# Kernel tuning notes

Hardware: AMD Instinct MI355X
Metric: run time of the kernel (lower is better)

The kernel has to match this reference:

```python
import jax, jax.numpy as jnp
import numpy as np

EPS = 1e-5
NEG_SLOPE = 0.01  # F.leaky_relu default


def setup_inputs() -> dict:
    key = jax.random.key(0)
    k1, k2, k3, k4 = jax.random.split(key, 4)
    N, F, H = 8192, 512, 2
    inputs = jax.random.normal(k1, (N, F), dtype=jnp.float32)
    adj = jnp.zeros((N, N), dtype=jnp.float32)  # accepted but unused by the module
    # torch Linear(F, F*H, bias=False): y = x @ W with W of shape [F, F*H]
    W = jax.random.normal(k2, (F, F * H), dtype=jnp.float32) * (1.0 / np.sqrt(F))
    a_w = jax.random.normal(k3, (1,), dtype=jnp.float32)  # Linear(1,1) weight
    a_b = jax.random.normal(k4, (1,), dtype=jnp.float32)  # Linear(1,1) bias
    return {"inputs": inputs, "adj": adj, "W": W, "a_w": a_w, "a_b": a_b}


def reference(inputs, adj, W, a_w, a_b):
    # Wh, Ws = chunk(inputs @ W, 2)
    WhWs = inputs @ W                       # [N, 2F]
    Wh, Ws = jnp.split(WhWs, 2, axis=-1)    # each [N, F]
    # bias = a(ones) = a_w * 1 + a_b  (constant scalar broadcast)
    bias = (a_w + a_b)[0]
    # dense attention: tanh(Wh + Ws + bias) @ Wh^T  -> [N, N]
    scores = jnp.tanh(Wh + Ws + bias) @ Wh.T
    attn = jax.nn.softmax(scores, axis=-1)  # [N, N]
    out = attn @ Wh + inputs                # [N, F] residual
    # training-mode batch norm over node dim, no affine
    mean = jnp.mean(out, axis=0)
    var = jnp.var(out, axis=0)
    out = (out - mean) * jax.lax.rsqrt(var + EPS)
    return jnp.where(out >= 0, out, NEG_SLOPE * out)
```

## Files before the change

kernel.cpp:

```cpp
#include <hip/hip_runtime.h>

using f32x4 = float    __attribute__((ext_vector_type(4)));
using f16x8 = _Float16 __attribute__((ext_vector_type(8)));
using f16x4 = _Float16 __attribute__((ext_vector_type(4)));

__device__ __forceinline__ void gload_lds16(const void* g, void* l) {
    __builtin_amdgcn_global_load_lds(
        (__attribute__((address_space(1))) void*)(void*)g,
        (__attribute__((address_space(3))) void*)l, 16, 0, 0);
}


__global__ __launch_bounds__(256) void k_cvt_x(
    const float* __restrict__ in, _Float16* __restrict__ out) {
    int i = (blockIdx.x * 256 + threadIdx.x) * 8;
    f32x4 a = *(const f32x4*)(in + i);
    f32x4 b = *(const f32x4*)(in + i + 4);
    f16x8 o;
    #pragma unroll
    for (int j = 0; j < 4; ++j) { o[j] = (_Float16)a[j]; o[j + 4] = (_Float16)b[j]; }
    *(f16x8*)(out + i) = o;
}

__global__ __launch_bounds__(256) void k_cvtT(
    const float* __restrict__ in, _Float16* __restrict__ out, int R, int C) {
    __shared__ _Float16 tile[32][33];
    int c0 = blockIdx.x * 32, r0 = blockIdx.y * 32;
    int tx = threadIdx.x & 31, ty = threadIdx.x >> 5;
    #pragma unroll
    for (int i = ty; i < 32; i += 8)
        tile[i][tx] = (_Float16)in[(size_t)(r0 + i) * C + c0 + tx];
    __syncthreads();
    #pragma unroll
    for (int i = ty; i < 32; i += 8)
        out[(size_t)(c0 + i) * R + r0 + tx] = tile[tx][i];
}

__global__ __launch_bounds__(512, 4) void k_gemm1f(
    const _Float16* __restrict__ A, const _Float16* __restrict__ Bt,
    _Float16* __restrict__ Whh, _Float16* __restrict__ T,
    _Float16* __restrict__ WhT,
    const float* __restrict__ aw, const float* __restrict__ ab) {
    __shared__ _Float16 As[128 * 32];
    __shared__ _Float16 B0s[64 * 32];
    __shared__ _Float16 B1s[64 * 32];
    const float bias = aw[0] + ab[0];
    const int row0 = blockIdx.y * 128, col0 = blockIdx.x * 64;
    const int tid = threadIdx.x, w = tid >> 6, lane = tid & 63;
    const int wm = w >> 2, wn = w & 3;
    const int lrow = lane & 15, quad = lane >> 4;
    const int r16 = lane >> 2;
    const int kc = (((lane & 3) - ((lane >> 3) & 3)) & 3) * 8;
    const int sq = ((quad + ((lrow >> 1) & 3)) & 3) * 8;
    f32x4 acc0[4] = {}, acc1[4] = {};
    for (int k0 = 0; k0 < 512; k0 += 32) {
        gload_lds16(A + (size_t)(row0 + w * 16 + r16) * 512 + k0 + kc,
                    As + w * 512);
        if (w < 4)
            gload_lds16(Bt + (size_t)(col0 + w * 16 + r16) * 512 + k0 + kc,
                        B0s + w * 512);
        else
            gload_lds16(Bt + (size_t)(col0 + 512 + (w - 4) * 16 + r16) * 512 + k0 + kc,
                        B1s + (w - 4) * 512);
        __syncthreads();
        f16x8 af[4], b0, b1;
        #pragma unroll
        for (int i = 0; i < 4; ++i)
            af[i] = *(const f16x8*)(As + (wm * 64 + i * 16 + lrow) * 32 + sq);
        b0 = *(const f16x8*)(B0s + (wn * 16 + lrow) * 32 + sq);
        b1 = *(const f16x8*)(B1s + (wn * 16 + lrow) * 32 + sq);
        #pragma unroll
        for (int mi = 0; mi < 4; ++mi) {
            acc0[mi] = __builtin_amdgcn_mfma_f32_16x16x32_f16(af[mi], b0, acc0[mi], 0, 0, 0);
            acc1[mi] = __builtin_amdgcn_mfma_f32_16x16x32_f16(af[mi], b1, acc1[mi], 0, 0, 0);
        }
        __syncthreads();
    }
    const int col = col0 + wn * 16 + lrow;
    #pragma unroll
    for (int mi = 0; mi < 4; ++mi) {
        int rowb = row0 + wm * 64 + mi * 16 + quad * 4;
        f16x4 pw;
        #pragma unroll
        for (int r = 0; r < 4; ++r) {
            float wh = acc0[mi][r];
            float tt = tanhf(wh + acc1[mi][r] + bias);
            Whh[(size_t)(rowb + r) * 512 + col] = (_Float16)wh;
            T[(size_t)(rowb + r) * 512 + col]   = (_Float16)tt;
            pw[r] = (_Float16)wh;
        }
        *(f16x4*)(WhT + (size_t)col * 8192 + rowb) = pw;
    }
}

__global__ __launch_bounds__(512, 4) void k_gemm2(
    const _Float16* __restrict__ A,
    const _Float16* __restrict__ Bt,
    _Float16* __restrict__ Cp,
    float* __restrict__ msP, float* __restrict__ lsP) {
    __shared__ _Float16 As[256 * 64];
    __shared__ _Float16 Bs[128 * 64];
    const int row0 = blockIdx.y * 256, col0 = blockIdx.x * 128;
    const int tid = threadIdx.x, w = tid >> 6, lane = tid & 63;
    const int wm = w >> 1, wn = w & 1;
    const int lrow = lane & 15, quad = lane >> 4;
    const int r8 = lane >> 3;
    const int kc8 = (((lane & 7) - r8) & 7) * 8;
    f32x4 acc[4][4] = {};
    for (int k0 = 0; k0 < 512; k0 += 64) {
        #pragma unroll
        for (int i = 0; i < 6; ++i) {
            int c = w + i * 8;
            if (c < 32) {
                gload_lds16(A + (size_t)(row0 + c * 8 + r8) * 512 + k0 + kc8,
                            As + c * 512);
            } else {
                int c2 = c - 32;
                gload_lds16(Bt + (size_t)(col0 + c2 * 8 + r8) * 512 + k0 + kc8,
                            Bs + c2 * 512);
            }
        }
        __syncthreads();
        #pragma unroll
        for (int ks = 0; ks < 2; ++ks) {
            const int sl = ((quad + ks * 4 + lrow) & 7) * 8;
            f16x8 af[4], bf[4];
            #pragma unroll
            for (int i = 0; i < 4; ++i)
                af[i] = *(const f16x8*)(As + (wm * 64 + i * 16 + lrow) * 64 + sl);
            #pragma unroll
            for (int i = 0; i < 4; ++i)
                bf[i] = *(const f16x8*)(Bs + (wn * 64 + i * 16 + lrow) * 64 + sl);
            #pragma unroll
            for (int mi = 0; mi < 4; ++mi)
                #pragma unroll
                for (int ni = 0; ni < 4; ++ni)
                    acc[mi][ni] = __builtin_amdgcn_mfma_f32_16x16x32_f16(
                        af[mi], bf[ni], acc[mi][ni], 0, 0, 0);
        }
        __syncthreads();
    }
    const int cb = blockIdx.x * 2 + wn;
    #pragma unroll
    for (int mi = 0; mi < 4; ++mi) {
        #pragma unroll
        for (int r = 0; r < 4; ++r) {
            const int row = row0 + wm * 64 + mi * 16 + quad * 4 + r;
            float vq[4]; float sm = -3.0e38f;
            #pragma unroll
            for (int ni = 0; ni < 4; ++ni) {
                _Float16 hv = (_Float16)acc[mi][ni][r];
                Cp[(size_t)row * 8192 + col0 + wn * 64 + ni * 16 + lrow] = hv;
                vq[ni] = (float)hv;
                sm = fmaxf(sm, vq[ni]);
            }
            #pragma unroll
            for (int off = 1; off < 16; off <<= 1)
                sm = fmaxf(sm, __shfl_xor(sm, off));
            float ls = 0.f;
            #pragma unroll
            for (int ni = 0; ni < 4; ++ni) ls += __expf(vq[ni] - sm);
            #pragma unroll
            for (int off = 1; off < 16; off <<= 1)
                ls += __shfl_xor(ls, off);
            if (lrow == 0) {
                msP[(size_t)cb * 8192 + row] = sm;
                lsP[(size_t)cb * 8192 + row] = ls;
            }
        }
    }
}

__global__ __launch_bounds__(64) void k_rowstats(
    const float* __restrict__ ms, const float* __restrict__ ls,
    float* __restrict__ mrow, float* __restrict__ rl) {
    const int row = blockIdx.x * 64 + threadIdx.x;
    float m[8], l[8];
    #pragma unroll
    for (int k = 0; k < 8; ++k) { m[k] = -3.0e38f; l[k] = 0.f; }
    for (int j = 0; j < 16; ++j) {
        #pragma unroll
        for (int k = 0; k < 8; ++k) {
            const int cb = k * 16 + j;
            float mb = ms[(size_t)cb * 8192 + row];
            float lb = ls[(size_t)cb * 8192 + row];
            float mn = fmaxf(m[k], mb);
            l[k] = l[k] * __expf(m[k] - mn) + lb * __expf(mb - mn);
            m[k] = mn;
        }
    }
    float M = m[0];
    #pragma unroll
    for (int k = 1; k < 8; ++k) M = fmaxf(M, m[k]);
    float L = 0.f;
    #pragma unroll
    for (int k = 0; k < 8; ++k) L += l[k] * __expf(m[k] - M);
    mrow[row] = M * 1.44269504f;
    rl[row]   = 1.f / L;
}

__global__ __launch_bounds__(512, 4) void k_gemm3(
    const _Float16* __restrict__ A,
    const _Float16* __restrict__ Bt,
    const float* __restrict__ mrow,
    float* __restrict__ Cp) {
    __shared__ _Float16 As[128 * 64];
    __shared__ _Float16 Bs[256 * 64];
    const int row0 = blockIdx.y * 128, col0 = blockIdx.x * 256;
    const size_t zoff = (size_t)blockIdx.z * 2048;
    Cp += (size_t)blockIdx.z * ((size_t)8192 * 512);
    const int tid = threadIdx.x, w = tid >> 6, lane = tid & 63;
    const int wm = w >> 2, wn = w & 3;
    const int lrow = lane & 15, quad = lane >> 4;
    const int r8 = lane >> 3;
    const int kc8 = (((lane & 7) - r8) & 7) * 8;
    const int rowA0 = row0 + w * 8 + r8;
    const int rowA1 = row0 + (w + 8) * 8 + r8;
    const float ms0 = mrow[rowA0];
    const float ms1 = mrow[rowA1];
    f32x4 acc[4][4] = {};
    for (int k0 = 0; k0 < 2048; k0 += 64) {
        f16x8 h0 = *(const f16x8*)(A + (size_t)rowA0 * 8192 + zoff + k0 + kc8);
        f16x8 h1 = *(const f16x8*)(A + (size_t)rowA1 * 8192 + zoff + k0 + kc8);
        f16x8 q0, q1;
        #pragma unroll
        for (int j = 0; j < 8; ++j) {
            q0[j] = (_Float16)exp2f(fmaf((float)h0[j], 1.44269504f, -ms0));
            q1[j] = (_Float16)exp2f(fmaf((float)h1[j], 1.44269504f, -ms1));
        }
        *(f16x8*)(As + w * 512 + lane * 8)       = q0;
        *(f16x8*)(As + (w + 8) * 512 + lane * 8) = q1;
        #pragma unroll
        for (int i = 2; i < 6; ++i) {
            int c2 = w + i * 8 - 16;
            gload_lds16(Bt + (size_t)(col0 + c2 * 8 + r8) * 8192 + zoff + k0 + kc8,
                        Bs + c2 * 512);
        }
        __syncthreads();
        #pragma unroll
        for (int ks = 0; ks < 2; ++ks) {
            const int sl = ((quad + ks * 4 + lrow) & 7) * 8;
            f16x8 af[4], bf[4];
            #pragma unroll
            for (int i = 0; i < 4; ++i)
                af[i] = *(const f16x8*)(As + (wm * 64 + i * 16 + lrow) * 64 + sl);
            #pragma unroll
            for (int i = 0; i < 4; ++i)
                bf[i] = *(const f16x8*)(Bs + (wn * 64 + i * 16 + lrow) * 64 + sl);
            #pragma unroll
            for (int mi = 0; mi < 4; ++mi)
                #pragma unroll
                for (int ni = 0; ni < 4; ++ni)
                    acc[mi][ni] = __builtin_amdgcn_mfma_f32_16x16x32_f16(
                        af[mi], bf[ni], acc[mi][ni], 0, 0, 0);
        }
        __syncthreads();
    }
    #pragma unroll
    for (int mi = 0; mi < 4; ++mi) {
        #pragma unroll
        for (int ni = 0; ni < 4; ++ni) {
            int col = col0 + wn * 64 + ni * 16 + lrow;
            #pragma unroll
            for (int r = 0; r < 4; ++r) {
                int row = row0 + wm * 64 + mi * 16 + quad * 4 + r;
                Cp[(size_t)row * 512 + col] = acc[mi][ni][r];
            }
        }
    }
}

__global__ __launch_bounds__(256) void k_reduce_stats(
    const float* __restrict__ part, const float* __restrict__ X,
    const float* __restrict__ rl,
    float* __restrict__ outf, float* __restrict__ cs, float* __restrict__ cq) {
    const int t = threadIdx.x;
    const int r0 = blockIdx.x * 32;
    constexpr size_t PS = (size_t)8192 * 512;
    float s0 = 0, q0 = 0, s1 = 0, q1 = 0;
    for (int r = 0; r < 32; ++r) {
        size_t base = (size_t)(r0 + r) * 512;
        float rlv = rl[r0 + r];
        float a = (part[base + t] + part[PS + base + t]
                + part[2 * PS + base + t] + part[3 * PS + base + t]) * rlv
                + X[base + t];
        float b = (part[base + t + 256] + part[PS + base + t + 256]
                + part[2 * PS + base + t + 256] + part[3 * PS + base + t + 256]) * rlv
                + X[base + t + 256];
        outf[base + t] = a;       outf[base + t + 256] = b;
        s0 += a; q0 += a * a; s1 += b; q1 += b * b;
    }
    atomicAdd(&cs[t], s0);       atomicAdd(&cq[t], q0);
    atomicAdd(&cs[t + 256], s1); atomicAdd(&cq[t + 256], q1);
}

__global__ __launch_bounds__(256) void k_bn_lrelu(
    const float* __restrict__ outf, const float* __restrict__ colsum,
    const float* __restrict__ colsq, float* __restrict__ out) {
    int i = blockIdx.x * 256 + threadIdx.x;
    int c = i & 511;
    constexpr float rN = 1.f / 8192.f;
    float mean = colsum[c] * rN;
    float var  = colsq[c] * rN - mean * mean;
    float y = (outf[i] - mean) * rsqrtf(var + 1e-5f);
    y = (y >= 0.f) ? y : 0.01f * y;
    out[i] = y;
}

extern "C" void kernel_launch(void* const* d_in, const int* in_sizes, int n_in,
                              void* d_out, int out_size, void* d_ws, size_t ws_size,
                              hipStream_t stream) {
    const float* X  = (const float*)d_in[0];
    const float* W  = (const float*)d_in[2];
    const float* aw = (const float*)d_in[3];
    const float* ab = (const float*)d_in[4];
    float* out = (float*)d_out;

    char* ws = (char*)d_ws;
    _Float16* Xh   = (_Float16*)(ws + 0x0);
    _Float16* Wt   = (_Float16*)(ws + 0x800000);
    _Float16* T    = (_Float16*)(ws + 0x900000);
    _Float16* Whh  = (_Float16*)(ws + 0x1100000);
    _Float16* WhT  = (_Float16*)(ws + 0x1900000);
    _Float16* S    = (_Float16*)(ws + 0x2100000);
    float*    outf = (float*)   (ws + 0xA100000);
    float*    part = (float*)   (ws + 0xB100000);
    float*    msP  = (float*)   (ws + 0xB100000);
    float*    lsP  = (float*)   (ws + 0xB500000);
    float*    cs   = (float*)   (ws + 0xF100000);
    float*    cq   = (float*)   (ws + 0xF100800);
    float*    mrow = (float*)   (ws + 0xF101000);
    float*    rl   = (float*)   (ws + 0xF109000);

    hipMemsetAsync(cs, 0, 4096, stream);
    k_cvt_x<<<dim3((8192 * 512) / 2048), 256, 0, stream>>>(X, Xh);
    k_cvtT<<<dim3(1024 / 32, 512 / 32), 256, 0, stream>>>(W, Wt, 512, 1024);
    k_gemm1f<<<dim3(8, 64), 512, 0, stream>>>(Xh, Wt, Whh, T, WhT, aw, ab);
    k_gemm2<<<dim3(64, 32), 512, 0, stream>>>(T, Whh, S, msP, lsP);
    k_rowstats<<<dim3(128), 64, 0, stream>>>(msP, lsP, mrow, rl);
    k_gemm3<<<dim3(2, 64, 4), 512, 0, stream>>>(S, WhT, mrow, part);
    k_reduce_stats<<<dim3(256), 256, 0, stream>>>(part, X, rl, outf, cs, cq);
    k_bn_lrelu<<<dim3((8192 * 512) / 256), 256, 0, stream>>>(outf, cs, cq, out);
}
```

Baseline: 535.7 us.

## Move softmax denominator accumulation into the PV GEMM and simplify row stats

The gemm2 epilogue now records only per-block row maxima and no longer computes or stores partial exp sums. A simpler k_rowmax kernel reduces those maxima. The softmax denominators are summed inside k_gemm3 from the exponentials it already computes, and reduce_stats inverts them. The change also remaps gemm3 to a 1D grid with a swizzled block order for better L2 locality, and issues the B-tile async loads before the A exp work to overlap them.

```diff
diff --git a/kernel.cpp b/kernel.cpp
--- a/kernel.cpp
+++ b/kernel.cpp
@@ -97,7 +97,7 @@
     const _Float16* __restrict__ A,
     const _Float16* __restrict__ Bt,
     _Float16* __restrict__ Cp,
-    float* __restrict__ msP, float* __restrict__ lsP) {
+    float* __restrict__ msP) {
     __shared__ _Float16 As[256 * 64];
     __shared__ _Float16 Bs[128 * 64];
     const int row0 = blockIdx.y * 256, col0 = blockIdx.x * 128;
@@ -146,69 +146,51 @@
         #pragma unroll
         for (int r = 0; r < 4; ++r) {
             const int row = row0 + wm * 64 + mi * 16 + quad * 4 + r;
-            float vq[4]; float sm = -3.0e38f;
+            float sm = -3.0e38f;
             #pragma unroll
             for (int ni = 0; ni < 4; ++ni) {
                 _Float16 hv = (_Float16)acc[mi][ni][r];
                 Cp[(size_t)row * 8192 + col0 + wn * 64 + ni * 16 + lrow] = hv;
-                vq[ni] = (float)hv;
-                sm = fmaxf(sm, vq[ni]);
+                sm = fmaxf(sm, (float)hv);
             }
             #pragma unroll
             for (int off = 1; off < 16; off <<= 1)
                 sm = fmaxf(sm, __shfl_xor(sm, off));
-            float ls = 0.f;
-            #pragma unroll
-            for (int ni = 0; ni < 4; ++ni) ls += __expf(vq[ni] - sm);
-            #pragma unroll
-            for (int off = 1; off < 16; off <<= 1)
-                ls += __shfl_xor(ls, off);
-            if (lrow == 0) {
-                msP[(size_t)cb * 8192 + row] = sm;
-                lsP[(size_t)cb * 8192 + row] = ls;
-            }
-        }
-    }
-}
-
-__global__ __launch_bounds__(64) void k_rowstats(
-    const float* __restrict__ ms, const float* __restrict__ ls,
-    float* __restrict__ mrow, float* __restrict__ rl) {
-    const int row = blockIdx.x * 64 + threadIdx.x;
-    float m[8], l[8];
-    #pragma unroll
-    for (int k = 0; k < 8; ++k) { m[k] = -3.0e38f; l[k] = 0.f; }
-    for (int j = 0; j < 16; ++j) {
-        #pragma unroll
-        for (int k = 0; k < 8; ++k) {
-            const int cb = k * 16 + j;
-            float mb = ms[(size_t)cb * 8192 + row];
-            float lb = ls[(size_t)cb * 8192 + row];
-            float mn = fmaxf(m[k], mb);
-            l[k] = l[k] * __expf(m[k] - mn) + lb * __expf(mb - mn);
-            m[k] = mn;
-        }
-    }
-    float M = m[0];
-    #pragma unroll
-    for (int k = 1; k < 8; ++k) M = fmaxf(M, m[k]);
-    float L = 0.f;
-    #pragma unroll
-    for (int k = 0; k < 8; ++k) L += l[k] * __expf(m[k] - M);
+            if (lrow == 0) msP[(size_t)cb * 8192 + row] = sm;
+        }
+    }
+}
+
+__global__ __launch_bounds__(256) void k_rowmax(
+    const float* __restrict__ ms, float* __restrict__ mrow) {
+    const int row = blockIdx.x * 256 + threadIdx.x;
+    float m[8];
+    #pragma unroll
+    for (int k = 0; k < 8; ++k) m[k] = -3.0e38f;
+    #pragma unroll
+    for (int j = 0; j < 16; ++j)
+        #pragma unroll
+        for (int k = 0; k < 8; ++k)
+            m[k] = fmaxf(m[k], ms[(size_t)(j * 8 + k) * 8192 + row]);
+    float M = fmaxf(fmaxf(fmaxf(m[0], m[1]), fmaxf(m[2], m[3])),
+                    fmaxf(fmaxf(m[4], m[5]), fmaxf(m[6], m[7])));
     mrow[row] = M * 1.44269504f;
-    rl[row]   = 1.f / L;
 }
 
 __global__ __launch_bounds__(512, 4) void k_gemm3(
     const _Float16* __restrict__ A,
     const _Float16* __restrict__ Bt,
     const float* __restrict__ mrow,
-    float* __restrict__ Cp) {
+    float* __restrict__ Cp,
+    float* __restrict__ lpart) {
     __shared__ _Float16 As[128 * 64];
     __shared__ _Float16 Bs[256 * 64];
-    const int row0 = blockIdx.y * 128, col0 = blockIdx.x * 256;
-    const size_t zoff = (size_t)blockIdx.z * 2048;
-    Cp += (size_t)blockIdx.z * ((size_t)8192 * 512);
+    const int bid = blockIdx.x;
+    const int orig = ((bid & 7) << 6) | (bid >> 3);
+    const int bx = orig & 1, by = (orig >> 1) & 63, bz = orig >> 7;
+    const int row0 = by * 128, col0 = bx * 256;
+    const size_t zoff = (size_t)bz * 2048;
+    Cp += (size_t)bz * ((size_t)8192 * 512);
     const int tid = threadIdx.x, w = tid >> 6, lane = tid & 63;
     const int wm = w >> 2, wn = w & 3;
     const int lrow = lane & 15, quad = lane >> 4;
@@ -218,24 +200,29 @@
     const int rowA1 = row0 + (w + 8) * 8 + r8;
     const float ms0 = mrow[rowA0];
     const float ms1 = mrow[rowA1];
+    float lsum0 = 0.f, lsum1 = 0.f;
     f32x4 acc[4][4] = {};
     for (int k0 = 0; k0 < 2048; k0 += 64) {
+        #pragma unroll
+        for (int i = 0; i < 4; ++i) {
+            int c2 = w + i * 8;
+            gload_lds16(Bt + (size_t)(col0 + c2 * 8 + r8) * 8192 + zoff + k0 + kc8,
+                        Bs + c2 * 512);
+        }
         f16x8 h0 = *(const f16x8*)(A + (size_t)rowA0 * 8192 + zoff + k0 + kc8);
         f16x8 h1 = *(const f16x8*)(A + (size_t)rowA1 * 8192 + zoff + k0 + kc8);
         f16x8 q0, q1;
+        float e0 = 0.f, e1 = 0.f;
         #pragma unroll
         for (int j = 0; j < 8; ++j) {
-            q0[j] = (_Float16)exp2f(fmaf((float)h0[j], 1.44269504f, -ms0));
-            q1[j] = (_Float16)exp2f(fmaf((float)h1[j], 1.44269504f, -ms1));
-        }
+            float a0 = exp2f(fmaf((float)h0[j], 1.44269504f, -ms0));
+            float a1 = exp2f(fmaf((float)h1[j], 1.44269504f, -ms1));
+            q0[j] = (_Float16)a0; q1[j] = (_Float16)a1;
+            e0 += a0; e1 += a1;
+        }
+        lsum0 += e0; lsum1 += e1;
         *(f16x8*)(As + w * 512 + lane * 8)       = q0;
         *(f16x8*)(As + (w + 8) * 512 + lane * 8) = q1;
-        #pragma unroll
-        for (int i = 2; i < 6; ++i) {
-            int c2 = w + i * 8 - 16;
-            gload_lds16(Bt + (size_t)(col0 + c2 * 8 + r8) * 8192 + zoff + k0 + kc8,
-                        Bs + c2 * 512);
-        }
         __syncthreads();
         #pragma unroll
         for (int ks = 0; ks < 2; ++ks) {
@@ -256,6 +243,17 @@
         }
         __syncthreads();
     }
+    if (bx == 0) {
+        #pragma unroll
+        for (int off = 1; off < 8; off <<= 1) {
+            lsum0 += __shfl_xor(lsum0, off);
+            lsum1 += __shfl_xor(lsum1, off);
+        }
+        if ((lane & 7) == 0) {
+            lpart[(size_t)bz * 8192 + rowA0] = lsum0;
+            lpart[(size_t)bz * 8192 + rowA1] = lsum1;
+        }
+    }
     #pragma unroll
     for (int mi = 0; mi < 4; ++mi) {
         #pragma unroll
@@ -272,7 +270,7 @@
 
 __global__ __launch_bounds__(256) void k_reduce_stats(
     const float* __restrict__ part, const float* __restrict__ X,
-    const float* __restrict__ rl,
+    const float* __restrict__ lpart,
     float* __restrict__ outf, float* __restrict__ cs, float* __restrict__ cq) {
     const int t = threadIdx.x;
     const int r0 = blockIdx.x * 32;
@@ -280,7 +278,8 @@
     float s0 = 0, q0 = 0, s1 = 0, q1 = 0;
     for (int r = 0; r < 32; ++r) {
         size_t base = (size_t)(r0 + r) * 512;
-        float rlv = rl[r0 + r];
+        float rlv = 1.f / (lpart[r0 + r] + lpart[8192 + r0 + r]
+                         + lpart[2 * 8192 + r0 + r] + lpart[3 * 8192 + r0 + r]);
         float a = (part[base + t] + part[PS + base + t]
                 + part[2 * PS + base + t] + part[3 * PS + base + t]) * rlv
                 + X[base + t];
@@ -326,19 +325,18 @@
     float*    outf = (float*)   (ws + 0xA100000);
     float*    part = (float*)   (ws + 0xB100000);
     float*    msP  = (float*)   (ws + 0xB100000);
-    float*    lsP  = (float*)   (ws + 0xB500000);
     float*    cs   = (float*)   (ws + 0xF100000);
     float*    cq   = (float*)   (ws + 0xF100800);
     float*    mrow = (float*)   (ws + 0xF101000);
-    float*    rl   = (float*)   (ws + 0xF109000);
+    float*    lpart= (float*)   (ws + 0xF109000);
 
     hipMemsetAsync(cs, 0, 4096, stream);
     k_cvt_x<<<dim3((8192 * 512) / 2048), 256, 0, stream>>>(X, Xh);
     k_cvtT<<<dim3(1024 / 32, 512 / 32), 256, 0, stream>>>(W, Wt, 512, 1024);
     k_gemm1f<<<dim3(8, 64), 512, 0, stream>>>(Xh, Wt, Whh, T, WhT, aw, ab);
-    k_gemm2<<<dim3(64, 32), 512, 0, stream>>>(T, Whh, S, msP, lsP);
-    k_rowstats<<<dim3(128), 64, 0, stream>>>(msP, lsP, mrow, rl);
-    k_gemm3<<<dim3(2, 64, 4), 512, 0, stream>>>(S, WhT, mrow, part);
-    k_reduce_stats<<<dim3(256), 256, 0, stream>>>(part, X, rl, outf, cs, cq);
+    k_gemm2<<<dim3(64, 32), 512, 0, stream>>>(T, Whh, S, msP);
+    k_rowmax<<<dim3(32), 256, 0, stream>>>(msP, mrow);
+    k_gemm3<<<dim3(512), 512, 0, stream>>>(S, WhT, mrow, part, lpart);
+    k_reduce_stats<<<dim3(256), 256, 0, stream>>>(part, X, lpart, outf, cs, cq);
     k_bn_lrelu<<<dim3((8192 * 512) / 256), 256, 0, stream>>>(outf, cs, cq, out);
 }
```

After: 538.4 us. Within noise of the previous version (+0.5%).
